# Kernel optimization log

Hardware: AMD Instinct MI355X
Metric: run time of the kernel (lower is better)

The kernel has to match this reference:

```python
import jax, jax.numpy as jnp
import numpy as np
from itertools import product

N = 120000      # active voxels
D = 128         # dense grid resolution per axis
CIN = 64
COUT = 64
K = 27          # 3x3x3 kernel volume
EPS = 1e-5


def setup_inputs() -> dict:
    # Build a random sparse voxel set and its kernel-offset neighbor map (torchsparse kmap).
    rng = np.random.default_rng(0)
    flat = rng.choice(D ** 3, size=N, replace=False)
    cz, cy, cx = np.unravel_index(flat, (D, D, D))
    coords = np.stack([cz, cy, cx], axis=1)               # [N, 3]
    lut = np.full(D ** 3, -1, dtype=np.int64)
    lut[flat] = np.arange(N)
    nbr = np.empty((K, N), dtype=np.int32)
    for k, (dz, dy, dx) in enumerate(product((-1, 0, 1), repeat=3)):
        nc = coords + np.array([dz, dy, dx])
        valid = np.all((nc >= 0) & (nc < D), axis=1)
        fl = np.ravel_multi_index(np.clip(nc, 0, D - 1).T, (D, D, D))
        nbr[k] = np.where(valid, lut[fl], -1).astype(np.int32)

    key = jax.random.key(0)
    k1, k2, k3, k4 = jax.random.split(key, 4)
    feats = jax.random.normal(k1, (N, CIN), dtype=jnp.float32)
    # torchsparse Conv3d weight layout: [kernel_volume, in_channels, out_channels]
    weight = jax.random.normal(k2, (K, CIN, COUT), dtype=jnp.float32) / np.float32(np.sqrt(K * CIN))
    gamma = jax.random.uniform(k3, (COUT,), dtype=jnp.float32, minval=0.5, maxval=1.5)
    beta = jax.random.normal(k4, (COUT,), dtype=jnp.float32) * 0.1
    return {"feats": feats, "weight": weight, "gamma": gamma, "beta": beta,
            "neighbor_idx": jnp.asarray(nbr)}


def reference(feats, weight, gamma, beta, neighbor_idx):
    # Sparse conv = gather -> per-offset matmul -> accumulate (stride 1, same voxel set).
    mask = (neighbor_idx >= 0)                      # [K, N]
    safe = jnp.maximum(neighbor_idx, 0)
    gathered = feats[safe] * mask[..., None]        # [K, N, Cin], missing neighbors zeroed
    out = jnp.einsum('knc,kcd->nd', gathered, weight)  # [N, Cout]
    # BatchNorm over active voxels (training-mode batch statistics), then ReLU.
    mean = out.mean(axis=0)
    var = out.var(axis=0)
    y = gamma * (out - mean) * jax.lax.rsqrt(var + EPS) + beta
    return jnp.maximum(y, 0.0)
```

## Files before the change

### kernel.cpp

```cpp
#include <hip/hip_runtime.h>

#define NVOX 120000
#define KVOL 27
#define CH 64
#define TOTAL (NVOX * CH)
#define NF4 (TOTAL / 4)
#define EPSV 1e-5f

typedef __attribute__((ext_vector_type(8))) short bf16x8;
typedef __attribute__((ext_vector_type(4))) float f32x4;

__device__ __forceinline__ unsigned short f2bf(float f) {
    unsigned int u = __builtin_bit_cast(unsigned int, f);
    u += 0x7FFFu + ((u >> 16) & 1u);
    return (unsigned short)(u >> 16);
}

__global__ void prep(const float* __restrict__ w, unsigned short* __restrict__ wtf,
                     float* __restrict__ stats) {
    const int b = blockIdx.x;
    const int tid = threadIdx.x;
    const int t = b * 256 + tid;
    const int d = t & 63, c = (t >> 6) & 63, k = t >> 12;
    const int grp = (d >> 4) * 2 + (c >> 5);
    const int l = ((c & 31) >> 3) * 16 + (d & 15);
    const int j = c & 7;
    wtf[(((size_t)k * 8 + grp) * 64 + l) * 8 + j] = f2bf(w[t]);
    if (b == 0 && tid < 128) stats[tid] = 0.f;
}

__device__ __forceinline__ void gatherRowF(const float* __restrict__ f,
                                           int idx, int q, bf16x8& a0, bf16x8& a1) {
    const int safe = idx < 0 ? 0 : idx;
    const float* row = f + (size_t)safe * CH + q * 8;
    const float4 p0 = *(const float4*)(row);
    const float4 p1 = *(const float4*)(row + 4);
    const float4 p2 = *(const float4*)(row + 32);
    const float4 p3 = *(const float4*)(row + 36);
    a0 = (bf16x8){(short)f2bf(p0.x), (short)f2bf(p0.y), (short)f2bf(p0.z), (short)f2bf(p0.w),
                  (short)f2bf(p1.x), (short)f2bf(p1.y), (short)f2bf(p1.z), (short)f2bf(p1.w)};
    a1 = (bf16x8){(short)f2bf(p2.x), (short)f2bf(p2.y), (short)f2bf(p2.z), (short)f2bf(p2.w),
                  (short)f2bf(p3.x), (short)f2bf(p3.y), (short)f2bf(p3.z), (short)f2bf(p3.w)};
    if (idx < 0) {
        a0 = (bf16x8)(short)0;
        a1 = (bf16x8)(short)0;
    }
}

__launch_bounds__(256, 3)
__global__ void conv_mfma(const float* __restrict__ feats,
                          const unsigned short* __restrict__ WtF,
                          const int* __restrict__ nbr,
                          float* __restrict__ out,
                          float* __restrict__ stats) {
    __shared__ float lstats[128];
    const int tid = threadIdx.x;
    const int lane = tid & 63;
    const int m = lane & 15;
    const int q = lane >> 4;
    const int v0 = blockIdx.x * 192 + (tid >> 6) * 48;
    const int r[3] = {v0 + m, v0 + 16 + m, v0 + 32 + m};

    f32x4 acc[3][4];
#pragma unroll
    for (int t = 0; t < 3; ++t)
#pragma unroll
        for (int nt = 0; nt < 4; ++nt)
            acc[t][nt] = (f32x4){0.f, 0.f, 0.f, 0.f};
    if (tid < 128) lstats[tid] = 0.f;
    __syncthreads();

    bf16x8 a[3][2];
    unsigned long long msk[3];
    int idxn[3];
#pragma unroll
    for (int t = 0; t < 3; ++t) {
        const int i = nbr[r[t]];
        msk[t] = __ballot(i >= 0);
        if (msk[t]) gatherRowF(feats, i, q, a[t][0], a[t][1]);
        else { a[t][0] = (bf16x8)(short)0; a[t][1] = (bf16x8)(short)0; }
        idxn[t] = nbr[NVOX + r[t]];
    }

    for (int k = 0; k < KVOL; ++k) {
        unsigned long long mn[3];
        bf16x8 an[3][2];
#pragma unroll
        for (int t = 0; t < 3; ++t) {
            mn[t] = __ballot(idxn[t] >= 0);
            if (mn[t]) gatherRowF(feats, idxn[t], q, an[t][0], an[t][1]);
        }
        int idxf[3] = {-1, -1, -1};
        if (k + 2 < KVOL) {
            const int* nb = nbr + (size_t)(k + 2) * NVOX;
#pragma unroll
            for (int t = 0; t < 3; ++t) idxf[t] = nb[r[t]];
        }

        if (msk[0] | msk[1] | msk[2]) {
            const unsigned short* wk = WtF + (size_t)k * 4096 + lane * 8;
            bf16x8 bfr[8];
#pragma unroll
            for (int h = 0; h < 8; ++h)
                bfr[h] = *(const bf16x8*)(wk + h * 512);
#pragma unroll
            for (int t = 0; t < 3; ++t) {
                if (msk[t]) {
#pragma unroll
                    for (int nt = 0; nt < 4; ++nt) {
                        acc[t][nt] = __builtin_amdgcn_mfma_f32_16x16x32_bf16(a[t][0], bfr[nt * 2 + 0], acc[t][nt], 0, 0, 0);
                        acc[t][nt] = __builtin_amdgcn_mfma_f32_16x16x32_bf16(a[t][1], bfr[nt * 2 + 1], acc[t][nt], 0, 0, 0);
                    }
                }
            }
        }

#pragma unroll
        for (int t = 0; t < 3; ++t) {
            a[t][0] = an[t][0];
            a[t][1] = an[t][1];
            msk[t] = mn[t];
            idxn[t] = idxf[t];
        }
    }

#pragma unroll
    for (int t = 0; t < 3; ++t) {
        float* ob = out + (size_t)(v0 + t * 16 + q * 4) * CH + m;
#pragma unroll
        for (int nt = 0; nt < 4; ++nt)
#pragma unroll
            for (int rr = 0; rr < 4; ++rr)
                ob[(size_t)rr * CH + nt * 16] = acc[t][nt][rr];
    }

#pragma unroll
    for (int nt = 0; nt < 4; ++nt) {
        float s = 0.f, s2 = 0.f;
#pragma unroll
        for (int t = 0; t < 3; ++t)
#pragma unroll
            for (int rr = 0; rr < 4; ++rr) {
                const float x = acc[t][nt][rr];
                s += x;
                s2 = fmaf(x, x, s2);
            }
        s  += __shfl_xor(s, 16);  s  += __shfl_xor(s, 32);
        s2 += __shfl_xor(s2, 16); s2 += __shfl_xor(s2, 32);
        if (lane < 16) {
            atomicAdd(&lstats[nt * 16 + m], s);
            atomicAdd(&lstats[64 + nt * 16 + m], s2);
        }
    }
    __syncthreads();
    if (tid < 128) atomicAdd(&stats[tid], lstats[tid]);
}

__launch_bounds__(256)
__global__ void bn_relu(float* __restrict__ out, const float* __restrict__ stats,
                        const float* __restrict__ gamma, const float* __restrict__ beta) {
    __shared__ float sb[128];
    const int tid = threadIdx.x;
    if (tid < 64) {
        const float inv_n = 1.0f / (float)NVOX;
        const float mean = stats[tid] * inv_n;
        const float var = stats[64 + tid] * inv_n - mean * mean;
        const float sc = gamma[tid] * rsqrtf(var + EPSV);
        sb[tid] = sc;
        sb[64 + tid] = beta[tid] - mean * sc;
    }
    __syncthreads();
    float4* o4 = (float4*)out;
    for (int e = blockIdx.x * 256 + tid; e < NF4; e += 960 * 256) {
        float4 x = o4[e];
        const int cb = (e & 15) * 4;
        x.x = fmaxf(fmaf(x.x, sb[cb + 0], sb[64 + cb + 0]), 0.f);
        x.y = fmaxf(fmaf(x.y, sb[cb + 1], sb[64 + cb + 1]), 0.f);
        x.z = fmaxf(fmaf(x.z, sb[cb + 2], sb[64 + cb + 2]), 0.f);
        x.w = fmaxf(fmaf(x.w, sb[cb + 3], sb[64 + cb + 3]), 0.f);
        o4[e] = x;
    }
}

extern "C" void kernel_launch(void* const* d_in, const int* in_sizes, int n_in,
                              void* d_out, int out_size, void* d_ws, size_t ws_size,
                              hipStream_t stream) {
    const float* feats  = (const float*)d_in[0];
    const float* weight = (const float*)d_in[1];
    const float* gamma  = (const float*)d_in[2];
    const float* beta   = (const float*)d_in[3];
    const int*   nbr    = (const int*)d_in[4];
    float* out = (float*)d_out;

    float* stats = (float*)d_ws;
    unsigned short* WtF = (unsigned short*)((char*)d_ws + 512);

    prep<<<432, 256, 0, stream>>>(weight, WtF, stats);
    conv_mfma<<<NVOX / 192, 256, 0, stream>>>(feats, WtF, nbr, out, stats);
    bn_relu<<<960, 256, 0, stream>>>(out, stats, gamma, beta);
}
```

Measured before the change: 157.4 us.

## Pre-convert features to bf16 with a zero row and shrink conv tiles

The prep kernel now also converts all input features to a bf16 copy in workspace and appends a zero row at index NVOX. The conv kernel gathers bf16 rows directly, so each gather moves half the bytes and skips the per-gather float-to-bf16 conversion; missing neighbours point at the zero row instead of branching. Each wave now handles 32 voxels instead of 48, launch bounds move to 4 blocks per SM, weights are loaded unconditionally each k, and bounds guards handle the last partial block. The cost is an extra full pass that reads feats and writes the bf16 copy, plus more blocks that each re-read the weights.

```diff
diff --git a/kernel.cpp b/kernel.cpp
--- a/kernel.cpp
+++ b/kernel.cpp
@@ -8,6 +8,7 @@
 #define EPSV 1e-5f
 
 typedef __attribute__((ext_vector_type(8))) short bf16x8;
+typedef __attribute__((ext_vector_type(8))) unsigned short u16x8;
 typedef __attribute__((ext_vector_type(4))) float f32x4;
 
 __device__ __forceinline__ unsigned short f2bf(float f) {
@@ -16,39 +17,35 @@
     return (unsigned short)(u >> 16);
 }
 
-__global__ void prep(const float* __restrict__ w, unsigned short* __restrict__ wtf,
+#define WBLK 432
+#define FBLK 3750
+__global__ void prep(const float* __restrict__ w, const float* __restrict__ feats,
+                     unsigned short* __restrict__ wtf, unsigned short* __restrict__ fb,
                      float* __restrict__ stats) {
     const int b = blockIdx.x;
     const int tid = threadIdx.x;
-    const int t = b * 256 + tid;
-    const int d = t & 63, c = (t >> 6) & 63, k = t >> 12;
-    const int grp = (d >> 4) * 2 + (c >> 5);
-    const int l = ((c & 31) >> 3) * 16 + (d & 15);
-    const int j = c & 7;
-    wtf[(((size_t)k * 8 + grp) * 64 + l) * 8 + j] = f2bf(w[t]);
-    if (b == 0 && tid < 128) stats[tid] = 0.f;
-}
-
-__device__ __forceinline__ void gatherRowF(const float* __restrict__ f,
-                                           int idx, int q, bf16x8& a0, bf16x8& a1) {
-    const int safe = idx < 0 ? 0 : idx;
-    const float* row = f + (size_t)safe * CH + q * 8;
-    const float4 p0 = *(const float4*)(row);
-    const float4 p1 = *(const float4*)(row + 4);
-    const float4 p2 = *(const float4*)(row + 32);
-    const float4 p3 = *(const float4*)(row + 36);
-    a0 = (bf16x8){(short)f2bf(p0.x), (short)f2bf(p0.y), (short)f2bf(p0.z), (short)f2bf(p0.w),
-                  (short)f2bf(p1.x), (short)f2bf(p1.y), (short)f2bf(p1.z), (short)f2bf(p1.w)};
-    a1 = (bf16x8){(short)f2bf(p2.x), (short)f2bf(p2.y), (short)f2bf(p2.z), (short)f2bf(p2.w),
-                  (short)f2bf(p3.x), (short)f2bf(p3.y), (short)f2bf(p3.z), (short)f2bf(p3.w)};
-    if (idx < 0) {
-        a0 = (bf16x8)(short)0;
-        a1 = (bf16x8)(short)0;
-    }
-}
-
-__launch_bounds__(256, 3)
-__global__ void conv_mfma(const float* __restrict__ feats,
+    if (b < WBLK) {
+        const int t = b * 256 + tid;
+        const int d = t & 63, c = (t >> 6) & 63, k = t >> 12;
+        const int grp = (d >> 4) * 2 + (c >> 5);
+        const int l = ((c & 31) >> 3) * 16 + (d & 15);
+        const int j = c & 7;
+        wtf[(((size_t)k * 8 + grp) * 64 + l) * 8 + j] = f2bf(w[t]);
+        if (b == 0 && tid < 128) stats[tid] = 0.f;
+        if (b == 1 && tid < 8) ((u16x8*)fb)[(size_t)NVOX * 8 + tid] = (u16x8)0;
+    } else {
+        const int t = (b - WBLK) * 256 + tid;
+        const float4* src = (const float4*)feats + (size_t)t * 2;
+        const float4 p0 = src[0];
+        const float4 p1 = src[1];
+        u16x8 v = {f2bf(p0.x), f2bf(p0.y), f2bf(p0.z), f2bf(p0.w),
+                   f2bf(p1.x), f2bf(p1.y), f2bf(p1.z), f2bf(p1.w)};
+        ((u16x8*)fb)[t] = v;
+    }
+}
+
+__launch_bounds__(256, 4)
+__global__ void conv_mfma(const unsigned short* __restrict__ FB,
                           const unsigned short* __restrict__ WtF,
                           const int* __restrict__ nbr,
                           float* __restrict__ out,
@@ -58,65 +55,70 @@
     const int lane = tid & 63;
     const int m = lane & 15;
     const int q = lane >> 4;
-    const int v0 = blockIdx.x * 192 + (tid >> 6) * 48;
-    const int r[3] = {v0 + m, v0 + 16 + m, v0 + 32 + m};
-
-    f32x4 acc[3][4];
-#pragma unroll
-    for (int t = 0; t < 3; ++t)
+    const int v0 = blockIdx.x * 128 + (tid >> 6) * 32;
+    const bool tv[2] = { v0 < NVOX, v0 + 16 < NVOX };
+    const int r[2] = { v0 + m, v0 + 16 + m };
+
+    f32x4 acc[2][4];
+#pragma unroll
+    for (int t = 0; t < 2; ++t)
 #pragma unroll
         for (int nt = 0; nt < 4; ++nt)
             acc[t][nt] = (f32x4){0.f, 0.f, 0.f, 0.f};
     if (tid < 128) lstats[tid] = 0.f;
     __syncthreads();
 
-    bf16x8 a[3][2];
-    unsigned long long msk[3];
-    int idxn[3];
-#pragma unroll
-    for (int t = 0; t < 3; ++t) {
-        const int i = nbr[r[t]];
+    const bf16x8* fbv = (const bf16x8*)FB;
+
+    bf16x8 a[2][2];
+    unsigned long long msk[2];
+    int idxn[2];
+#pragma unroll
+    for (int t = 0; t < 2; ++t) {
+        const int i = tv[t] ? nbr[r[t]] : -1;
         msk[t] = __ballot(i >= 0);
-        if (msk[t]) gatherRowF(feats, i, q, a[t][0], a[t][1]);
-        else { a[t][0] = (bf16x8)(short)0; a[t][1] = (bf16x8)(short)0; }
-        idxn[t] = nbr[NVOX + r[t]];
+        const bf16x8* row = fbv + (size_t)(i < 0 ? NVOX : i) * 8;
+        a[t][0] = row[q];
+        a[t][1] = row[q + 4];
+        idxn[t] = tv[t] ? nbr[NVOX + r[t]] : -1;
     }
 
     for (int k = 0; k < KVOL; ++k) {
-        unsigned long long mn[3];
-        bf16x8 an[3][2];
-#pragma unroll
-        for (int t = 0; t < 3; ++t) {
+        const unsigned short* wk = WtF + (size_t)k * 4096 + lane * 8;
+        bf16x8 bfr[8];
+#pragma unroll
+        for (int h = 0; h < 8; ++h)
+            bfr[h] = *(const bf16x8*)(wk + h * 512);
+
+        unsigned long long mn[2];
+        bf16x8 an[2][2];
+#pragma unroll
+        for (int t = 0; t < 2; ++t) {
             mn[t] = __ballot(idxn[t] >= 0);
-            if (mn[t]) gatherRowF(feats, idxn[t], q, an[t][0], an[t][1]);
-        }
-        int idxf[3] = {-1, -1, -1};
+            const bf16x8* row = fbv + (size_t)(idxn[t] < 0 ? NVOX : idxn[t]) * 8;
+            an[t][0] = row[q];
+            an[t][1] = row[q + 4];
+        }
+        int idxf[2] = {-1, -1};
         if (k + 2 < KVOL) {
             const int* nb = nbr + (size_t)(k + 2) * NVOX;
 #pragma unroll
-            for (int t = 0; t < 3; ++t) idxf[t] = nb[r[t]];
-        }
-
-        if (msk[0] | msk[1] | msk[2]) {
-            const unsigned short* wk = WtF + (size_t)k * 4096 + lane * 8;
-            bf16x8 bfr[8];
-#pragma unroll
-            for (int h = 0; h < 8; ++h)
-                bfr[h] = *(const bf16x8*)(wk + h * 512);
-#pragma unroll
-            for (int t = 0; t < 3; ++t) {
-                if (msk[t]) {
-#pragma unroll
-                    for (int nt = 0; nt < 4; ++nt) {
-                        acc[t][nt] = __builtin_amdgcn_mfma_f32_16x16x32_bf16(a[t][0], bfr[nt * 2 + 0], acc[t][nt], 0, 0, 0);
-                        acc[t][nt] = __builtin_amdgcn_mfma_f32_16x16x32_bf16(a[t][1], bfr[nt * 2 + 1], acc[t][nt], 0, 0, 0);
-                    }
+            for (int t = 0; t < 2; ++t) idxf[t] = tv[t] ? nb[r[t]] : -1;
+        }
+
+#pragma unroll
+        for (int t = 0; t < 2; ++t) {
+            if (msk[t]) {
+#pragma unroll
+                for (int nt = 0; nt < 4; ++nt) {
+                    acc[t][nt] = __builtin_amdgcn_mfma_f32_16x16x32_bf16(a[t][0], bfr[nt * 2 + 0], acc[t][nt], 0, 0, 0);
+                    acc[t][nt] = __builtin_amdgcn_mfma_f32_16x16x32_bf16(a[t][1], bfr[nt * 2 + 1], acc[t][nt], 0, 0, 0);
                 }
             }
         }
 
 #pragma unroll
-        for (int t = 0; t < 3; ++t) {
+        for (int t = 0; t < 2; ++t) {
             a[t][0] = an[t][0];
             a[t][1] = an[t][1];
             msk[t] = mn[t];
@@ -125,20 +127,22 @@
     }
 
 #pragma unroll
-    for (int t = 0; t < 3; ++t) {
-        float* ob = out + (size_t)(v0 + t * 16 + q * 4) * CH + m;
-#pragma unroll
-        for (int nt = 0; nt < 4; ++nt)
-#pragma unroll
-            for (int rr = 0; rr < 4; ++rr)
-                ob[(size_t)rr * CH + nt * 16] = acc[t][nt][rr];
+    for (int t = 0; t < 2; ++t) {
+        if (tv[t]) {
+            float* ob = out + (size_t)(v0 + t * 16 + q * 4) * CH + m;
+#pragma unroll
+            for (int nt = 0; nt < 4; ++nt)
+#pragma unroll
+                for (int rr = 0; rr < 4; ++rr)
+                    ob[(size_t)rr * CH + nt * 16] = acc[t][nt][rr];
+        }
     }
 
 #pragma unroll
     for (int nt = 0; nt < 4; ++nt) {
         float s = 0.f, s2 = 0.f;
 #pragma unroll
-        for (int t = 0; t < 3; ++t)
+        for (int t = 0; t < 2; ++t)
 #pragma unroll
             for (int rr = 0; rr < 4; ++rr) {
                 const float x = acc[t][nt][rr];
@@ -194,8 +198,9 @@
 
     float* stats = (float*)d_ws;
     unsigned short* WtF = (unsigned short*)((char*)d_ws + 512);
-
-    prep<<<432, 256, 0, stream>>>(weight, WtF, stats);
-    conv_mfma<<<NVOX / 192, 256, 0, stream>>>(feats, WtF, nbr, out, stats);
+    unsigned short* FB  = (unsigned short*)((char*)d_ws + 512 + 221184);
+
+    prep<<<WBLK + FBLK, 256, 0, stream>>>(weight, feats, WtF, FB, stats);
+    conv_mfma<<<(NVOX + 127) / 128, 256, 0, stream>>>(FB, WtF, nbr, out, stats);
     bn_relu<<<960, 256, 0, stream>>>(out, stats, gamma, beta);
 }
```

Measured after the change: 163.1 us. 3.6% more time.
